# Kernel tuning notes

Hardware: AMD Instinct MI355X
Metric: run time of the kernel (lower is better)

## Reference

```python
import jax, jax.numpy as jnp
import numpy as np

B, C, K, D_SUB = 32768, 32, 256, 16
D_IN, D_OUT = C * D_SUB, 512


def setup_inputs() -> dict:
    key = jax.random.key(0)
    k1, k2, k3 = jax.random.split(key, 3)
    inputs = jax.random.normal(k1, (B, C, D_SUB), dtype=jnp.float32)
    centroids = jax.random.normal(k2, (C, K, D_SUB), dtype=jnp.float32)
    W = jax.random.normal(k3, (D_IN, D_OUT), dtype=jnp.float32) * (1.0 / np.sqrt(D_IN))
    return {"inputs": inputs, "centroids": centroids, "W": W}


def reference(inputs, centroids, W):
    # dot-metric response: (B, C, K). Equivalent to
    # torch.matmul(inputs.transpose(0,1), centroids.transpose(1,2)).transpose(0,1)
    response = jnp.einsum('bcd,ckd->bck', inputs, centroids)
    neg_mse = jnp.max(response, axis=-1)            # (B, C)
    codes = jnp.argmax(response, axis=-1)           # (B, C) int
    # codebook gather: outputs[b,c] = centroids[c, codes[b,c]]
    outputs = centroids[jnp.arange(C), codes]       # (B, C, D_SUB)
    # tie_in_n_out straight-through: value equals `outputs` in forward
    product = outputs.reshape(-1, C * D_SUB) @ W    # (B, D_OUT); fc has no bias
    return product, -neg_mse, codes
```

## Files before the change

### kernel.cpp

```cpp
#include <hip/hip_runtime.h>


#define NB 32768
#define NC 32
#define NK 256
#define NDS 16
#define NDIN 512
#define NDOUT 512
#define CERT 0.008f

typedef __attribute__((ext_vector_type(8))) short s8v;
typedef __attribute__((ext_vector_type(4))) float f4v;
typedef __attribute__((ext_vector_type(4))) unsigned int u4v;

__device__ __forceinline__ unsigned short f2bf(float f) {
  unsigned int u = __float_as_uint(f);
  u += 0x7fffu + ((u >> 16) & 1u);
  return (unsigned short)(u >> 16);
}
__device__ __forceinline__ float bf2f(unsigned short h) {
  return __uint_as_float(((unsigned int)h) << 16);
}

#define CVTPK(d, lo, hi) \
  asm("v_cvt_pk_bf16_f32 %0, %1, %2" : "=v"(d) : "v"(lo), "v"(hi))

__device__ __forceinline__ void gload16(const void* g, void* l) {
  __builtin_amdgcn_global_load_lds(
      (const __attribute__((address_space(1))) void*)g,
      (__attribute__((address_space(3))) void*)l, 16, 0, 0);
}

__device__ __forceinline__ float dot16(const float* x, const float* cj) {
  float4 a0 = *(const float4*)(x + 0),  a1 = *(const float4*)(x + 4);
  float4 a2 = *(const float4*)(x + 8),  a3 = *(const float4*)(x + 12);
  float4 c0 = *(const float4*)(cj + 0), c1 = *(const float4*)(cj + 4);
  float4 c2 = *(const float4*)(cj + 8), c3 = *(const float4*)(cj + 12);
  float s = a0.x * c0.x;
  s = fmaf(a0.y, c0.y, s); s = fmaf(a0.z, c0.z, s); s = fmaf(a0.w, c0.w, s);
  s = fmaf(a1.x, c1.x, s); s = fmaf(a1.y, c1.y, s); s = fmaf(a1.z, c1.z, s); s = fmaf(a1.w, c1.w, s);
  s = fmaf(a2.x, c2.x, s); s = fmaf(a2.y, c2.y, s); s = fmaf(a2.z, c2.z, s); s = fmaf(a2.w, c2.w, s);
  s = fmaf(a3.x, c3.x, s); s = fmaf(a3.y, c3.y, s); s = fmaf(a3.z, c3.z, s); s = fmaf(a3.w, c3.w, s);
  return s;
}

__global__ __launch_bounds__(256) void k_prep(const float* __restrict__ W,
                                              const float* __restrict__ cents,
                                              unsigned short* __restrict__ Wt,
                                              unsigned short* __restrict__ centsH,
                                              unsigned short* __restrict__ centsP4) {
  const int t = threadIdx.x;
  const int bid = blockIdx.x;
  if (bid < 256) {
    __shared__ float tile[32][33];
    const int k0 = (bid >> 4) << 5;
    const int n0 = (bid & 15) << 5;
    const int tx = t & 31, ty = t >> 5;
#pragma unroll
    for (int i = 0; i < 4; ++i) {
      int r = ty + i * 8;
      tile[r][tx] = W[(size_t)(k0 + r) * NDOUT + n0 + tx];
    }
    __syncthreads();
#pragma unroll
    for (int i = 0; i < 4; ++i) {
      int r = ty + i * 8;
      Wt[(size_t)(n0 + r) * NDIN + k0 + tx] = f2bf(tile[tx][r]);
    }
  } else {
    const int c = bid - 256;
    const int k = t;
    const float* src = cents + ((size_t)c * NK + k) * NDS;
    unsigned short hi[16], lo[16];
#pragma unroll
    for (int j = 0; j < 4; ++j) {
      float4 v = *(const float4*)(src + j * 4);
      unsigned short h0 = f2bf(v.x), h1 = f2bf(v.y), h2 = f2bf(v.z), h3 = f2bf(v.w);
      hi[j * 4 + 0] = h0; hi[j * 4 + 1] = h1; hi[j * 4 + 2] = h2; hi[j * 4 + 3] = h3;
      lo[j * 4 + 0] = f2bf(v.x - bf2f(h0));
      lo[j * 4 + 1] = f2bf(v.y - bf2f(h1));
      lo[j * 4 + 2] = f2bf(v.z - bf2f(h2));
      lo[j * 4 + 3] = f2bf(v.w - bf2f(h3));
    }
    unsigned short* hf = centsH + ((size_t)c * NK + k) * NDS;
#pragma unroll
    for (int j = 0; j < 4; ++j)
      *(ushort4*)(hf + j * 4) = make_ushort4(hi[j * 4], hi[j * 4 + 1], hi[j * 4 + 2], hi[j * 4 + 3]);
    unsigned short* pb = centsP4 + (size_t)c * 8192 + k * 8;
    *(ushort4*)(pb + 0 * 2048 + 0) = make_ushort4(hi[0], hi[1], hi[2], hi[3]);
    *(ushort4*)(pb + 0 * 2048 + 4) = make_ushort4(hi[4], hi[5], hi[6], hi[7]);
    *(ushort4*)(pb + 1 * 2048 + 0) = make_ushort4(hi[8], hi[9], hi[10], hi[11]);
    *(ushort4*)(pb + 1 * 2048 + 4) = make_ushort4(hi[12], hi[13], hi[14], hi[15]);
    *(ushort4*)(pb + 2 * 2048 + 0) = make_ushort4(lo[0], lo[1], lo[2], lo[3]);
    *(ushort4*)(pb + 2 * 2048 + 4) = make_ushort4(lo[4], lo[5], lo[6], lo[7]);
    *(ushort4*)(pb + 3 * 2048 + 0) = make_ushort4(lo[8], lo[9], lo[10], lo[11]);
    *(ushort4*)(pb + 3 * 2048 + 4) = make_ushort4(lo[12], lo[13], lo[14], lo[15]);
  }
}

__device__ __forceinline__ void split8(float4 u0, float4 u1, s8v& bh, s8v& bl) {
  unsigned int ph0, ph1, ph2, ph3;
  CVTPK(ph0, u0.x, u0.y); CVTPK(ph1, u0.z, u0.w);
  CVTPK(ph2, u1.x, u1.y); CVTPK(ph3, u1.z, u1.w);
  bh = __builtin_bit_cast(s8v, (u4v){ph0, ph1, ph2, ph3});
  float ra = u0.x - __uint_as_float(ph0 << 16);
  float rb = u0.y - __uint_as_float(ph0 & 0xFFFF0000u);
  float rc = u0.z - __uint_as_float(ph1 << 16);
  float rd = u0.w - __uint_as_float(ph1 & 0xFFFF0000u);
  float re = u1.x - __uint_as_float(ph2 << 16);
  float rf = u1.y - __uint_as_float(ph2 & 0xFFFF0000u);
  float rg = u1.z - __uint_as_float(ph3 << 16);
  float rh = u1.w - __uint_as_float(ph3 & 0xFFFF0000u);
  unsigned int pl0, pl1, pl2, pl3;
  CVTPK(pl0, ra, rb); CVTPK(pl1, rc, rd);
  CVTPK(pl2, re, rf); CVTPK(pl3, rg, rh);
  bl = __builtin_bit_cast(s8v, (u4v){pl0, pl1, pl2, pl3});
}

#define TRACK2(v0, v1, kc0, best, sec, bk)                     \
  {                                                            \
    float vm_ = fmaxf(v0, v1);                                 \
    float md_ = __builtin_amdgcn_fmed3f(best, v0, v1);         \
    sec = fmaxf(sec, md_);                                     \
    int km_ = (v1 > v0) ? (kc0 + 1) : (kc0);                   \
    bool gt_ = vm_ > best;                                     \
    bk = gt_ ? km_ : bk;                                       \
    best = fmaxf(best, vm_);                                   \
  }

__global__ __launch_bounds__(256, 4) void k_score(const float* __restrict__ inputs,
                                                  const unsigned short* __restrict__ centsP4,
                                                  const float* __restrict__ cents,
                                                  float* __restrict__ T_neg,
                                                  int* __restrict__ T_code) {
  const int t = threadIdx.x;
  const int l = t & 63;
  const int w = t >> 6;
  const int c = blockIdx.y;
  const int b0 = blockIdx.x * 128 + w * 32;
  const int g = l >> 4;
  const int col = l & 15;
  const int dh = (g & 1) * 8;
  const int g4 = g * 4;

  const unsigned short* abase = centsP4 + (size_t)c * 8192 + g * 2048 + col * 8;
  s8v areg[16];
#pragma unroll
  for (int kt = 0; kt < 16; ++kt)
    areg[kt] = *(const s8v*)(abase + kt * 128);

  s8v bh0, bl0, bh1, bl1;
  {
    const float* r0 = inputs + ((size_t)(b0 + col) * NC + c) * NDS + dh;
    const float* r1 = inputs + ((size_t)(b0 + 16 + col) * NC + c) * NDS + dh;
    float4 u0 = *(const float4*)(r0), u1 = *(const float4*)(r0 + 4);
    float4 v0 = *(const float4*)(r1), v1 = *(const float4*)(r1 + 4);
    split8(u0, u1, bh0, bl0);
    split8(v0, v1, bh1, bl1);
    const s8v zer = {0, 0, 0, 0, 0, 0, 0, 0};
    if (l >= 32) { bl0 = zer; bl1 = zer; }
  }

  float best0 = -3.0e38f, sec0 = -3.0e38f;
  float best1 = -3.0e38f, sec1 = -3.0e38f;
  int bk0 = 0, bk1 = 0;
  const f4v zz = {0.0f, 0.0f, 0.0f, 0.0f};

#pragma unroll
  for (int kt = 0; kt < 16; ++kt) {
    s8v a = areg[kt];
    f4v acc0 = __builtin_amdgcn_mfma_f32_16x16x32_bf16(a, bh0, zz, 0, 0, 0);
    acc0 = __builtin_amdgcn_mfma_f32_16x16x32_bf16(a, bl0, acc0, 0, 0, 0);
    f4v acc1 = __builtin_amdgcn_mfma_f32_16x16x32_bf16(a, bh1, zz, 0, 0, 0);
    acc1 = __builtin_amdgcn_mfma_f32_16x16x32_bf16(a, bl1, acc1, 0, 0, 0);
    const int kc = kt * 16;
    TRACK2(acc0[0], acc0[1], kc + 0, best0, sec0, bk0)
    TRACK2(acc0[2], acc0[3], kc + 2, best0, sec0, bk0)
    TRACK2(acc1[0], acc1[1], kc + 0, best1, sec1, bk1)
    TRACK2(acc1[2], acc1[3], kc + 2, best1, sec1, bk1)
  }

  bk0 += g4;
  bk1 += g4;

#pragma unroll
  for (int off = 16; off <= 32; off <<= 1) {
    float vb = __shfl_xor(best0, off);
    float sb = __shfl_xor(sec0, off);
    int kb = __shfl_xor(bk0, off);
    float mn = fminf(best0, vb);
    sec0 = fmaxf(fmaxf(sec0, sb), mn);
    bool take = (vb > best0) || (vb == best0 && kb < bk0);
    bk0 = take ? kb : bk0;
    best0 = fmaxf(best0, vb);

    vb = __shfl_xor(best1, off);
    sb = __shfl_xor(sec1, off);
    kb = __shfl_xor(bk1, off);
    mn = fminf(best1, vb);
    sec1 = fmaxf(fmaxf(sec1, sb), mn);
    take = (vb > best1) || (vb == best1 && kb < bk1);
    bk1 = take ? kb : bk1;
    best1 = fmaxf(best1, vb);
  }

  const int sub = (l >> 4) & 1;
  float best = sub ? best1 : best0;
  float sec = sub ? sec1 : sec0;
  int bk = sub ? bk1 : bk0;
  const bool owner = (l < 32);
  const bool flagged = owner && (best - sec <= CERT);

  if (owner && !flagged) {
    const int b = b0 + l;
    const float* xr = inputs + ((size_t)b * NC + c) * NDS;
    const float* cr = cents + ((size_t)c * NK + bk) * NDS;
    size_t o = (size_t)c * NB + b;
    T_neg[o] = dot16(xr, cr);
    T_code[o] = bk;
  }

  unsigned long long mask = __ballot(flagged);
  while (mask) {
    const int p = __builtin_ctzll(mask);
    mask &= mask - 1;
    const int b = b0 + p;
    const float* xr = inputs + ((size_t)b * NC + c) * NDS;
    const float* cr = cents + ((size_t)c * NK + l * 4) * NDS;
    float rb = -3.0e38f;
    int rk = 0;
#pragma unroll
    for (int q = 0; q < 4; ++q) {
      float d = dot16(xr, cr + q * NDS);
      if (d > rb) { rb = d; rk = l * 4 + q; }
    }
#pragma unroll
    for (int off = 1; off <= 32; off <<= 1) {
      float vb = __shfl_xor(rb, off);
      int kb = __shfl_xor(rk, off);
      bool take = (vb > rb) || (vb == rb && kb < rk);
      rb = take ? vb : rb;
      rk = take ? kb : rk;
    }
    if (l == 0) {
      size_t o = (size_t)c * NB + b;
      T_neg[o] = rb;
      T_code[o] = rk;
    }
  }
}

__global__ __launch_bounds__(256) void k_finish(const float* __restrict__ T_neg,
                                                const int* __restrict__ T_code,
                                                float* __restrict__ negout,
                                                float* __restrict__ codefout,
                                                int* __restrict__ codeint) {
  __shared__ float sneg[64][33];
  __shared__ int scode[64][33];
  const int t = threadIdx.x;
  const int b0 = blockIdx.x * 64;

#pragma unroll
  for (int it = 0; it < 8; ++it) {
    int lin = it * 256 + t;
    int c = lin >> 6, bi = lin & 63;
    sneg[bi][c] = T_neg[(size_t)c * NB + b0 + bi];
    scode[bi][c] = T_code[(size_t)c * NB + b0 + bi];
  }
  __syncthreads();

#pragma unroll
  for (int it = 0; it < 8; ++it) {
    int lin = it * 256 + t;
    int bi = lin >> 5, c = lin & 31;
    size_t o = (size_t)(b0 + bi) * NC + c;
    int code = scode[bi][c];
    negout[o] = -sneg[bi][c];
    codefout[o] = (float)code;
    codeint[o] = code;
  }
}

__global__ __launch_bounds__(256) void k_gemm(const unsigned short* __restrict__ centsB,
                                              const int* __restrict__ codeint,
                                              const unsigned short* __restrict__ Wt,
                                              float* __restrict__ out) {
  __shared__ __align__(16) unsigned short As[128 * 64];
  __shared__ __align__(16) unsigned short Bs[128 * 64];
  __shared__ int lcode[128 * 33];

  const int t = threadIdx.x;
  const int l = t & 63;
  const int w = t >> 6;
  const int wm = w >> 1, wn = w & 1;
  const int m0 = blockIdx.x * 128;
  const int n0 = blockIdx.y * 128;

  {
    const int4* cp = (const int4*)(codeint + (size_t)m0 * NC);
#pragma unroll
    for (int i = 0; i < 4; ++i) {
      int idx = t + i * 256;
      int4 v = cp[idx];
      int row = idx >> 3, col = (idx & 7) * 4;
      lcode[row * 33 + col + 0] = v.x;
      lcode[row * 33 + col + 1] = v.y;
      lcode[row * 33 + col + 2] = v.z;
      lcode[row * 33 + col + 3] = v.w;
    }
  }

  f4v acc[4][4] = {};
  const int s = t & 7;
  const int rq = t >> 3;

  for (int kt = 0; kt < 8; ++kt) {
    __syncthreads();
    const int c0 = kt * 4;
#pragma unroll
    for (int i = 0; i < 4; ++i) {
      int lr = i * 32 + rq;
      int srcslot = s ^ (lr & 7);
      int cl = srcslot >> 1, half = srcslot & 1;
      int code = lcode[lr * 33 + c0 + cl];
      const unsigned short* gsrc =
          centsB + ((size_t)((c0 + cl) * NK + code) * NDS + half * 8);
      gload16(gsrc, (char*)As + i * 4096 + (w << 10));
    }
#pragma unroll
    for (int i = 0; i < 4; ++i) {
      int lr = i * 32 + rq;
      int k16 = s ^ (lr & 7);
      const unsigned short* gsrc = Wt + (size_t)(n0 + lr) * NDIN + kt * 64 + k16 * 8;
      gload16(gsrc, (char*)Bs + i * 4096 + (w << 10));
    }
    __syncthreads();

    s8v af[4][2], bfr[4][2];
#pragma unroll
    for (int mf = 0; mf < 4; ++mf)
#pragma unroll
      for (int ks = 0; ks < 2; ++ks) {
        int row = wm * 64 + mf * 16 + (l & 15);
        int slot = ks * 4 + (l >> 4);
        af[mf][ks] = *(const s8v*)((const char*)As + row * 128 + ((slot ^ (row & 7)) << 4));
      }
#pragma unroll
    for (int nf = 0; nf < 4; ++nf)
#pragma unroll
      for (int ks = 0; ks < 2; ++ks) {
        int row = wn * 64 + nf * 16 + (l & 15);
        int slot = ks * 4 + (l >> 4);
        bfr[nf][ks] = *(const s8v*)((const char*)Bs + row * 128 + ((slot ^ (row & 7)) << 4));
      }
#pragma unroll
    for (int ks = 0; ks < 2; ++ks)
#pragma unroll
      for (int mf = 0; mf < 4; ++mf)
#pragma unroll
        for (int nf = 0; nf < 4; ++nf)
          acc[mf][nf] = __builtin_amdgcn_mfma_f32_16x16x32_bf16(
              af[mf][ks], bfr[nf][ks], acc[mf][nf], 0, 0, 0);
  }

#pragma unroll
  for (int mf = 0; mf < 4; ++mf)
#pragma unroll
    for (int nf = 0; nf < 4; ++nf)
#pragma unroll
      for (int r = 0; r < 4; ++r) {
        int row = m0 + wm * 64 + mf * 16 + (l >> 4) * 4 + r;
        int col = n0 + wn * 64 + nf * 16 + (l & 15);
        out[(size_t)row * NDOUT + col] = acc[mf][nf][r];
      }
}

extern "C" void kernel_launch(void* const* d_in, const int* in_sizes, int n_in,
                              void* d_out, int out_size, void* d_ws, size_t ws_size,
                              hipStream_t stream) {
  const float* inputs = (const float*)d_in[0];
  const float* cents  = (const float*)d_in[1];
  const float* W      = (const float*)d_in[2];

  float* out = (float*)d_out;
  float* negout   = out + (size_t)NB * NDOUT;
  float* codefout = negout + (size_t)NB * NC;

  unsigned short* Wt      = (unsigned short*)d_ws;
  unsigned short* centsH  = (unsigned short*)((char*)d_ws + 512 * 1024);
  unsigned short* centsP4 = (unsigned short*)((char*)d_ws + (1 << 20));
  int* codeint            = (int*)((char*)d_ws + 2 * (1 << 20));
  float* T_neg            = (float*)((char*)d_ws + 6 * (1 << 20));
  int* T_code             = (int*)((char*)d_ws + 10 * (1 << 20));

  k_prep<<<288, 256, 0, stream>>>(W, cents, Wt, centsH, centsP4);
  k_score<<<dim3(NB / 128, NC), 256, 0, stream>>>(inputs, centsP4, cents, T_neg, T_code);
  k_finish<<<NB / 64, 256, 0, stream>>>(T_neg, T_code, negout, codefout, codeint);
  k_gemm<<<dim3(NB / 128, NDOUT / 128), 256, 0, stream>>>(centsH, codeint, Wt, out);
}
```

Measured before the change: 111.2 us.

## Use full hi/lo split in score MFMA and read codes directly in GEMM

The score kernel now feeds both the high and low bf16 parts of the inputs to all lanes by swapping them between lane halves, instead of zeroing the low part on half the lanes. This makes the bf16 dot product more accurate, so the certainty threshold for the fallback recheck is tightened from 0.008 to 0.004, with the aim of triggering fewer exact fp32 rechecks. The finish kernel no longer writes a separate int code buffer. The GEMM instead gathers codes straight from the channel-major T_code scratch with transposed loads, which removes one 4 MB write and its read-back at the cost of a less contiguous load pattern.

```diff
diff --git a/kernel.cpp b/kernel.cpp
--- a/kernel.cpp
+++ b/kernel.cpp
@@ -7,7 +7,7 @@
 #define NDS 16
 #define NDIN 512
 #define NDOUT 512
-#define CERT 0.008f
+#define CERT 0.004f
 
 typedef __attribute__((ext_vector_type(8))) short s8v;
 typedef __attribute__((ext_vector_type(4))) float f4v;
@@ -149,16 +149,20 @@
   for (int kt = 0; kt < 16; ++kt)
     areg[kt] = *(const s8v*)(abase + kt * 128);
 
-  s8v bh0, bl0, bh1, bl1;
+  s8v p1f0, p2f0, p1f1, p2f1;
   {
     const float* r0 = inputs + ((size_t)(b0 + col) * NC + c) * NDS + dh;
     const float* r1 = inputs + ((size_t)(b0 + 16 + col) * NC + c) * NDS + dh;
     float4 u0 = *(const float4*)(r0), u1 = *(const float4*)(r0 + 4);
     float4 v0 = *(const float4*)(r1), v1 = *(const float4*)(r1 + 4);
+    s8v bh0, bl0, bh1, bl1;
     split8(u0, u1, bh0, bl0);
     split8(v0, v1, bh1, bl1);
-    const s8v zer = {0, 0, 0, 0, 0, 0, 0, 0};
-    if (l >= 32) { bl0 = zer; bl1 = zer; }
+    const bool hiLane = (l < 32);
+    p1f0 = hiLane ? bh0 : bl0;
+    p2f0 = hiLane ? bl0 : bh0;
+    p1f1 = hiLane ? bh1 : bl1;
+    p2f1 = hiLane ? bl1 : bh1;
   }
 
   float best0 = -3.0e38f, sec0 = -3.0e38f;
@@ -169,10 +173,10 @@
 #pragma unroll
   for (int kt = 0; kt < 16; ++kt) {
     s8v a = areg[kt];
-    f4v acc0 = __builtin_amdgcn_mfma_f32_16x16x32_bf16(a, bh0, zz, 0, 0, 0);
-    acc0 = __builtin_amdgcn_mfma_f32_16x16x32_bf16(a, bl0, acc0, 0, 0, 0);
-    f4v acc1 = __builtin_amdgcn_mfma_f32_16x16x32_bf16(a, bh1, zz, 0, 0, 0);
-    acc1 = __builtin_amdgcn_mfma_f32_16x16x32_bf16(a, bl1, acc1, 0, 0, 0);
+    f4v acc0 = __builtin_amdgcn_mfma_f32_16x16x32_bf16(a, p1f0, zz, 0, 0, 0);
+    acc0 = __builtin_amdgcn_mfma_f32_16x16x32_bf16(a, p2f0, acc0, 0, 0, 0);
+    f4v acc1 = __builtin_amdgcn_mfma_f32_16x16x32_bf16(a, p1f1, zz, 0, 0, 0);
+    acc1 = __builtin_amdgcn_mfma_f32_16x16x32_bf16(a, p2f1, acc1, 0, 0, 0);
     const int kc = kt * 16;
     TRACK2(acc0[0], acc0[1], kc + 0, best0, sec0, bk0)
     TRACK2(acc0[2], acc0[3], kc + 2, best0, sec0, bk0)
@@ -253,8 +257,7 @@
 __global__ __launch_bounds__(256) void k_finish(const float* __restrict__ T_neg,
                                                 const int* __restrict__ T_code,
                                                 float* __restrict__ negout,
-                                                float* __restrict__ codefout,
-                                                int* __restrict__ codeint) {
+                                                float* __restrict__ codefout) {
   __shared__ float sneg[64][33];
   __shared__ int scode[64][33];
   const int t = threadIdx.x;
@@ -274,15 +277,13 @@
     int lin = it * 256 + t;
     int bi = lin >> 5, c = lin & 31;
     size_t o = (size_t)(b0 + bi) * NC + c;
-    int code = scode[bi][c];
     negout[o] = -sneg[bi][c];
-    codefout[o] = (float)code;
-    codeint[o] = code;
+    codefout[o] = (float)scode[bi][c];
   }
 }
 
 __global__ __launch_bounds__(256) void k_gemm(const unsigned short* __restrict__ centsB,
-                                              const int* __restrict__ codeint,
+                                              const int* __restrict__ T_code,
                                               const unsigned short* __restrict__ Wt,
                                               float* __restrict__ out) {
   __shared__ __align__(16) unsigned short As[128 * 64];
@@ -297,16 +298,16 @@
   const int n0 = blockIdx.y * 128;
 
   {
-    const int4* cp = (const int4*)(codeint + (size_t)m0 * NC);
+    const int cc = t >> 3;
+    const int ch = t & 7;
 #pragma unroll
     for (int i = 0; i < 4; ++i) {
-      int idx = t + i * 256;
-      int4 v = cp[idx];
-      int row = idx >> 3, col = (idx & 7) * 4;
-      lcode[row * 33 + col + 0] = v.x;
-      lcode[row * 33 + col + 1] = v.y;
-      lcode[row * 33 + col + 2] = v.z;
-      lcode[row * 33 + col + 3] = v.w;
+      int row0 = ch * 16 + i * 4;
+      int4 v = *(const int4*)(T_code + (size_t)cc * NB + m0 + row0);
+      lcode[(row0 + 0) * 33 + cc] = v.x;
+      lcode[(row0 + 1) * 33 + cc] = v.y;
+      lcode[(row0 + 2) * 33 + cc] = v.z;
+      lcode[(row0 + 3) * 33 + cc] = v.w;
     }
   }
 
@@ -389,12 +390,11 @@
   unsigned short* Wt      = (unsigned short*)d_ws;
   unsigned short* centsH  = (unsigned short*)((char*)d_ws + 512 * 1024);
   unsigned short* centsP4 = (unsigned short*)((char*)d_ws + (1 << 20));
-  int* codeint            = (int*)((char*)d_ws + 2 * (1 << 20));
-  float* T_neg            = (float*)((char*)d_ws + 6 * (1 << 20));
-  int* T_code             = (int*)((char*)d_ws + 10 * (1 << 20));
+  float* T_neg            = (float*)((char*)d_ws + 2 * (1 << 20));
+  int* T_code             = (int*)((char*)d_ws + 6 * (1 << 20));
 
   k_prep<<<288, 256, 0, stream>>>(W, cents, Wt, centsH, centsP4);
   k_score<<<dim3(NB / 128, NC), 256, 0, stream>>>(inputs, centsP4, cents, T_neg, T_code);
-  k_finish<<<NB / 64, 256, 0, stream>>>(T_neg, T_code, negout, codefout, codeint);
-  k_gemm<<<dim3(NB / 128, NDOUT / 128), 256, 0, stream>>>(centsH, codeint, Wt, out);
-}
+  k_finish<<<NB / 64, 256, 0, stream>>>(T_neg, T_code, negout, codefout);
+  k_gemm<<<dim3(NB / 128, NDOUT / 128), 256, 0, stream>>>(centsH, T_code, Wt, out);
+}
```

After: 104.8 us. 5.7% less time.
